# Kernel tuning notes

Hardware: AMD Instinct MI355X
Metric: run time of the kernel (lower is better)

The kernel has to match this reference:

```python
import jax, jax.numpy as jnp
import numpy as np

LN_EPS = 1e-5


def setup_inputs() -> dict:
    key = jax.random.key(0)
    k1, k2, k3 = jax.random.split(key, 3)
    B, T, D, H = 16, 512, 512, 1024
    x = jax.random.normal(k1, (B, T, D), dtype=jnp.float32)
    # nn.Linear weights: W in R^{2H x D}, U in R^{2H x H} (kaiming-ish scale)
    W_w = jax.random.normal(k2, (2 * H, D), dtype=jnp.float32) * (1.0 / np.sqrt(D))
    U_w = jax.random.normal(k3, (2 * H, H), dtype=jnp.float32) * (1.0 / np.sqrt(H))
    ln_gamma = jnp.ones((2 * H,), dtype=jnp.float32)
    ln_beta = jnp.zeros((2 * H,), dtype=jnp.float32)
    h0 = jnp.zeros((1, H), dtype=jnp.float32)
    return {"x": x, "W_w": W_w, "U_w": U_w, "ln_gamma": ln_gamma,
            "ln_beta": ln_beta, "h0": h0}


def _layernorm(w, gamma, beta):
    mu = jnp.mean(w, axis=-1, keepdims=True)
    var = jnp.mean(jnp.square(w - mu), axis=-1, keepdims=True)
    return (w - mu) * jax.lax.rsqrt(var + LN_EPS) * gamma + beta


def reference(x, W_w, U_w, ln_gamma, ln_beta, h0):
    # Input projection: w = x @ W^T -> [B, T, 2H], then LayerNorm over 2H
    w = jnp.einsum('btd,gd->btg', x, W_w)
    w = _layernorm(w, ln_gamma, ln_beta)

    B = x.shape[0]
    H = U_w.shape[1]
    ht0 = jnp.broadcast_to(h0, (B, H))
    U_t = U_w.T  # [H, 2H]

    def step(ht, wt):  # wt: [B, 2H]
        gates = wt + ht @ U_t
        at, zt = jnp.split(gates, 2, axis=1)
        zt = jax.nn.sigmoid(zt)
        hcand = jax.nn.relu(at)  # drop_mask = 1.0 in eval mode
        ht = zt * ht + (1.0 - zt) * hcand
        return ht, ht

    _, hs = jax.lax.scan(step, ht0, jnp.swapaxes(w, 0, 1))  # hs: [T, B, H]
    return jnp.swapaxes(hs, 0, 1)  # [B, T, H]
```

## Files before the change

kernel.cpp:

```cpp
#include <hip/hip_runtime.h>
#include <hip/hip_cooperative_groups.h>
#include <cmath>

typedef __bf16 bf16x8 __attribute__((ext_vector_type(8)));
typedef float floatx4 __attribute__((ext_vector_type(4)));
typedef unsigned ux4 __attribute__((ext_vector_type(4)));
typedef unsigned short u16;

#define B_ 16
#define T_ 512
#define D_ 512
#define H_ 1024
#define G_ 2048
#define BH (B_ * H_)
#define HP 1032

__global__ void cast_f32_bf16(const float* __restrict__ src, u16* __restrict__ dst, int n) {
  int i = blockIdx.x * blockDim.x + threadIdx.x;
  int stride = gridDim.x * blockDim.x;
  for (; i < n; i += stride) {
    __bf16 b = (__bf16)src[i];
    dst[i] = *reinterpret_cast<u16*>(&b);
  }
}

__launch_bounds__(256, 1)
__global__ void gemm_xW(const u16* __restrict__ xb, const u16* __restrict__ Wb,
                        float* __restrict__ w) {
  const int lane = threadIdx.x & 63;
  const int wv = threadIdx.x >> 6;
  const int rt0 = blockIdx.x * 16;
  const int bidx = rt0 >> 9;
  const int t0 = rt0 & 511;
  const int am = lane & 15;
  const int kq = lane >> 4;

  bf16x8 af[16];
  {
    const u16* xrow = xb + (size_t)(rt0 + am) * D_ + kq * 8;
#pragma unroll
    for (int kk = 0; kk < 16; ++kk)
      af[kk] = *reinterpret_cast<const bf16x8*>(xrow + kk * 32);
  }

#pragma unroll 1
  for (int nt = 0; nt < 32; ++nt) {
    const int n0 = wv * 512 + nt * 16;
    floatx4 acc = {0.f, 0.f, 0.f, 0.f};
    const u16* wrow = Wb + (size_t)(n0 + am) * D_ + kq * 8;
#pragma unroll
    for (int kk = 0; kk < 16; ++kk) {
      bf16x8 bfr = *reinterpret_cast<const bf16x8*>(wrow + kk * 32);
      acc = __builtin_amdgcn_mfma_f32_16x16x32_bf16(af[kk], bfr, acc, 0, 0, 0);
    }
#pragma unroll
    for (int i = 0; i < 4; ++i) {
      int m = kq * 4 + i;
      w[(size_t)((t0 + m) * 16 + bidx) * G_ + n0 + am] = acc[i];
    }
  }
}

__launch_bounds__(256, 1)
__global__ void layernorm_rows(float* __restrict__ w, const float* __restrict__ gamma,
                               const float* __restrict__ beta) {
  float* r = w + (size_t)blockIdx.x * G_;
  float v[8];
  float s = 0.f, ss = 0.f;
#pragma unroll
  for (int i = 0; i < 8; ++i) {
    v[i] = r[threadIdx.x + i * 256];
    s += v[i];
    ss += v[i] * v[i];
  }
#pragma unroll
  for (int d = 1; d < 64; d <<= 1) {
    s += __shfl_xor(s, d, 64);
    ss += __shfl_xor(ss, d, 64);
  }
  __shared__ float ls[4], lss[4];
  const int wv = threadIdx.x >> 6;
  if ((threadIdx.x & 63) == 0) { ls[wv] = s; lss[wv] = ss; }
  __syncthreads();
  float S = ls[0] + ls[1] + ls[2] + ls[3];
  float SS = lss[0] + lss[1] + lss[2] + lss[3];
  float mu = S * (1.f / 2048.f);
  float var = SS * (1.f / 2048.f) - mu * mu;
  float rs = rsqrtf(var + 1e-5f);
#pragma unroll
  for (int i = 0; i < 8; ++i) {
    int g = threadIdx.x + i * 256;
    r[g] = (v[i] - mu) * rs * gamma[g] + beta[g];
  }
}

__launch_bounds__(512, 1)
__global__ void ligru_scan(const float* __restrict__ w, const u16* __restrict__ Ub,
                           const float* __restrict__ h0, float* __restrict__ out,
                           unsigned* __restrict__ hbuf) {
  const int tid = threadIdx.x;
  const int lane = tid & 63;
  const int wv = tid >> 6;
  const int am = lane & 15;
  const int kq = lane >> 4;
  const int blk = blockIdx.x;
  const int j0 = blk * 32;
  const int jt = wv >> 1;
  const int kh = wv & 1;

  __shared__ u16 lds_h[16 * HP];
  __shared__ float lds_r[4][2][16][16];

  for (int i = tid; i < 8 * HP; i += 512) lds_h[8 * HP + i] = 0;

  const int grow = (am < 8) ? (j0 + 8 * jt + am) : (H_ + j0 + 8 * jt + (am - 8));

  bf16x8 uf[16];
  {
    const u16* urow = Ub + (size_t)grow * H_ + kh * 512 + kq * 8;
#pragma unroll
    for (int kk = 0; kk < 16; ++kk)
      uf[kk] = *reinterpret_cast<const bf16x8*>(urow + kk * 32);
  }

  const int ub = tid >> 5;
  const int jj = tid & 31;
  const int col = j0 + jj;
  const int scol = 4 * (tid & 255);
  const int sb = tid >> 8;
  float hreg = h0[col];
  float wa = __builtin_nontemporal_load(&w[(size_t)ub * G_ + col]);
  float wz = __builtin_nontemporal_load(&w[(size_t)ub * G_ + H_ + col]);

  {
    __bf16 hb = (__bf16)hreg;
    unsigned pk = ((unsigned)*reinterpret_cast<u16*>(&hb) << 16) | 1u;
    unsigned* pp = hbuf + ub * H_ + col;
    asm volatile("global_store_dword %0, %1, off sc0 sc1"
                 :: "v"(pp), "v"(pk) : "memory");
  }

  ux4 chv[4];
#define ISSUE_BUNDLE(base)                                                   \
  do {                                                                       \
    const unsigned* b_ = (base) + 4 * tid;                                   \
    asm volatile("global_load_dwordx4 %0, %4, off sc0 sc1\n\t"               \
                 "global_load_dwordx4 %1, %5, off sc0 sc1\n\t"               \
                 "global_load_dwordx4 %2, %6, off sc0 sc1\n\t"               \
                 "global_load_dwordx4 %3, %7, off sc0 sc1"                   \
                 : "=&v"(chv[0]), "=&v"(chv[1]), "=&v"(chv[2]), "=&v"(chv[3])\
                 : "v"(b_), "v"(b_ + 2048), "v"(b_ + 4096), "v"(b_ + 6144)   \
                 : "memory");                                                \
  } while (0)

  ISSUE_BUNDLE(hbuf);

  for (int t = 0; t < T_; ++t) {
    const unsigned tag = (unsigned)(t + 1);
#pragma unroll 1
    for (int g = 0; g < 2; ++g) {
      asm volatile("s_waitcnt vmcnt(0)"
                   : "+v"(chv[0]), "+v"(chv[1]), "+v"(chv[2]), "+v"(chv[3])
                   :: "memory");
      __builtin_amdgcn_sched_barrier(0);
      unsigned bad = 0;
#pragma unroll
      for (int c = 0; c < 4; ++c)
        bad |= ((chv[c].x ^ tag) | (chv[c].y ^ tag) |
                (chv[c].z ^ tag) | (chv[c].w ^ tag)) & 0xFFFFu;
      if (bad) {
        const unsigned* cb = hbuf + (size_t)(t & 1) * BH + g * 8192 + 4 * tid;
        unsigned rounds = 0;
        do {
          asm volatile(
              "global_load_dwordx4 %0, %4, off sc0 sc1\n\t"
              "global_load_dwordx4 %1, %5, off sc0 sc1\n\t"
              "global_load_dwordx4 %2, %6, off sc0 sc1\n\t"
              "global_load_dwordx4 %3, %7, off sc0 sc1\n\t"
              "s_waitcnt vmcnt(0)"
              : "=&v"(chv[0]), "=&v"(chv[1]), "=&v"(chv[2]), "=&v"(chv[3])
              : "v"(cb), "v"(cb + 2048), "v"(cb + 4096), "v"(cb + 6144)
              : "memory");
          bad = 0;
#pragma unroll
          for (int c = 0; c < 4; ++c)
            bad |= ((chv[c].x ^ tag) | (chv[c].y ^ tag) |
                    (chv[c].z ^ tag) | (chv[c].w ^ tag)) & 0xFFFFu;
        } while (bad && ++rounds < 2048u);
      }

#pragma unroll
      for (int c = 0; c < 4; ++c) {
        int b = 2 * c + sb;
        unsigned lo = (chv[c].x >> 16) | (chv[c].y & 0xFFFF0000u);
        unsigned hi = (chv[c].z >> 16) | (chv[c].w & 0xFFFF0000u);
        uint2 pk; pk.x = lo; pk.y = hi;
        *reinterpret_cast<uint2*>(&lds_h[b * HP + scol]) = pk;
      }
      asm volatile("s_waitcnt lgkmcnt(0)" ::: "memory");
      __builtin_amdgcn_s_barrier();
      __builtin_amdgcn_sched_barrier(0);

      floatx4 acc0 = {0, 0, 0, 0}, acc1 = {0, 0, 0, 0};
      {
        const u16* hb = &lds_h[am * HP + kh * 512 + kq * 8];
#pragma unroll
        for (int kk = 0; kk < 8; ++kk) {
          bf16x8 x0 = *reinterpret_cast<const bf16x8*>(hb + (kk + 0) * 32);
          bf16x8 x1 = *reinterpret_cast<const bf16x8*>(hb + (kk + 8) * 32);
          acc0 = __builtin_amdgcn_mfma_f32_16x16x32_bf16(x0, uf[kk + 0], acc0, 0, 0, 0);
          acc1 = __builtin_amdgcn_mfma_f32_16x16x32_bf16(x1, uf[kk + 8], acc1, 0, 0, 0);
        }
      }
      floatx4 acc = acc0 + acc1;

#pragma unroll
      for (int i = 0; i < 4; ++i)
        lds_r[jt][kh][kq * 4 + i][am] = acc[i];
      asm volatile("s_waitcnt lgkmcnt(0)" ::: "memory");
      __builtin_amdgcn_s_barrier();
      __builtin_amdgcn_sched_barrier(0);

      float wan = wa, wzn = wz;
      if (sb == g) {
        const int tl = jj >> 3, cc = jj & 7;
        const int mr = ub & 7;
        float a = lds_r[tl][0][mr][cc] + lds_r[tl][1][mr][cc] + wa;
        float z = lds_r[tl][0][mr][8 + cc] + lds_r[tl][1][mr][8 + cc] + wz;
        float zs = 1.f / (1.f + __expf(-z));
        float hn = zs * hreg + (1.f - zs) * fmaxf(a, 0.f);
        hreg = hn;
        __bf16 hb16 = (__bf16)hn;
        unsigned pk = ((unsigned)*reinterpret_cast<u16*>(&hb16) << 16) | (tag + 1u);
        unsigned* pp = hbuf + (size_t)((t + 1) & 1) * BH + ub * H_ + col;
        asm volatile("global_store_dword %0, %1, off sc0 sc1"
                     :: "v"(pp), "v"(pk) : "memory");
        __builtin_nontemporal_store(hn, &out[((size_t)ub * T_ + t) * H_ + col]);
        int tn = (t + 1 < T_) ? (t + 1) : t;
        const float* wt = w + (size_t)(tn * 16 + ub) * G_;
        wan = __builtin_nontemporal_load(&wt[col]);
        wzn = __builtin_nontemporal_load(&wt[H_ + col]);
      }
      wa = wan; wz = wzn;

      {
        int ntx = (g == 1) ? (t + 1) : t;
        const unsigned* nb = hbuf + (size_t)(ntx & 1) * BH + (g ^ 1) * 8192;
        ISSUE_BUNDLE(nb);
      }
    }
  }
#undef ISSUE_BUNDLE
}

extern "C" void kernel_launch(void* const* d_in, const int* in_sizes, int n_in,
                              void* d_out, int out_size, void* d_ws, size_t ws_size,
                              hipStream_t stream) {
  (void)in_sizes; (void)n_in; (void)out_size; (void)ws_size;
  const float* x = (const float*)d_in[0];
  const float* Ww = (const float*)d_in[1];
  const float* Uw = (const float*)d_in[2];
  const float* gamma = (const float*)d_in[3];
  const float* beta = (const float*)d_in[4];
  const float* h0 = (const float*)d_in[5];
  float* out = (float*)d_out;

  char* p = (char*)d_ws;
  u16* xb = (u16*)p;      p += (size_t)8192 * 512 * 2;
  u16* Wb = (u16*)p;      p += (size_t)2048 * 512 * 2;
  u16* Ub = (u16*)p;      p += (size_t)2048 * 1024 * 2;
  float* w = (float*)p;   p += (size_t)8192 * 2048 * 4;
  unsigned* hbuf = (unsigned*)p; p += (size_t)2 * BH * 4;

  hipMemsetAsync(hbuf, 0, (size_t)2 * BH * 4, stream);
  cast_f32_bf16<<<512, 256, 0, stream>>>(x, xb, 8192 * 512);
  cast_f32_bf16<<<256, 256, 0, stream>>>(Ww, Wb, 2048 * 512);
  cast_f32_bf16<<<256, 256, 0, stream>>>(Uw, Ub, 2048 * 1024);
  gemm_xW<<<512, 256, 0, stream>>>(xb, Wb, w);
  layernorm_rows<<<8192, 256, 0, stream>>>(w, gamma, beta);

  const float* wc = w;
  const u16* Ubc = Ub;
  void* args[5] = { (void*)&wc, (void*)&Ubc, (void*)&h0, (void*)&out, (void*)&hbuf };
  hipLaunchCooperativeKernel((void*)ligru_scan, dim3(32), dim3(512), args, 0, stream);
}
```

Measured before the change: 1.752 ms.

## Pin scan workgroups to one XCC and use L2-coherent polling loads

Launches 256 workgroups and elects the first XCC that gathers 32 of them to run the recurrent scan, while the other workgroups exit. With all 32 workers on one XCC, the h exchange can poll with sc0-only loads through the shared L2 instead of system-coherent sc0 sc1 loads. It falls back to sc0 sc1 loads after repeated stale reads. It also double-buffers the prefetch of w and issues it before the MFMA phase. The risk is that correctness of the sc0-only path depends on XCC co-location, and the election adds a startup cost plus extra launched blocks.

```diff
diff --git a/kernel.cpp b/kernel.cpp
--- a/kernel.cpp
+++ b/kernel.cpp
@@ -97,13 +97,28 @@
 __launch_bounds__(512, 1)
 __global__ void ligru_scan(const float* __restrict__ w, const u16* __restrict__ Ub,
                            const float* __restrict__ h0, float* __restrict__ out,
-                           unsigned* __restrict__ hbuf) {
+                           unsigned* __restrict__ hbuf, unsigned* __restrict__ elect) {
+  __shared__ unsigned s_role;
+  if (threadIdx.x == 0) {
+    unsigned xcc;
+    asm volatile("s_getreg_b32 %0, hwreg(HW_REG_XCC_ID)" : "=s"(xcc));
+    xcc &= 7u;
+    unsigned ticket = atomicAdd(&elect[xcc], 1u);
+    if (ticket == 31u) atomicCAS(&elect[8], 0u, xcc + 1u);
+    unsigned wn;
+    while ((wn = atomicAdd(&elect[8], 0u)) == 0u) __builtin_amdgcn_s_sleep(8);
+    s_role = (wn == xcc + 1u && ticket < 32u) ? ticket : 0xFFFFFFFFu;
+  }
+  __syncthreads();
+  const unsigned role = s_role;
+  if (role == 0xFFFFFFFFu) return;
+
   const int tid = threadIdx.x;
   const int lane = tid & 63;
   const int wv = tid >> 6;
   const int am = lane & 15;
   const int kq = lane >> 4;
-  const int blk = blockIdx.x;
+  const int blk = (int)role;
   const int j0 = blk * 32;
   const int jt = wv >> 1;
   const int kh = wv & 1;
@@ -129,8 +144,9 @@
   const int scol = 4 * (tid & 255);
   const int sb = tid >> 8;
   float hreg = h0[col];
-  float wa = __builtin_nontemporal_load(&w[(size_t)ub * G_ + col]);
-  float wz = __builtin_nontemporal_load(&w[(size_t)ub * G_ + H_ + col]);
+  float wa0 = __builtin_nontemporal_load(&w[(size_t)ub * G_ + col]);
+  float wz0 = __builtin_nontemporal_load(&w[(size_t)ub * G_ + H_ + col]);
+  float wa1 = 0.f, wz1 = 0.f;
 
   {
     __bf16 hb = (__bf16)hreg;
@@ -141,7 +157,19 @@
   }
 
   ux4 chv[4];
-#define ISSUE_BUNDLE(base)                                                   \
+  unsigned strikes = 0;
+#define ISSUE_SC0(base)                                                      \
+  do {                                                                       \
+    const unsigned* b_ = (base) + 4 * tid;                                   \
+    asm volatile("global_load_dwordx4 %0, %4, off sc0\n\t"                   \
+                 "global_load_dwordx4 %1, %5, off sc0\n\t"                   \
+                 "global_load_dwordx4 %2, %6, off sc0\n\t"                   \
+                 "global_load_dwordx4 %3, %7, off sc0"                       \
+                 : "=&v"(chv[0]), "=&v"(chv[1]), "=&v"(chv[2]), "=&v"(chv[3])\
+                 : "v"(b_), "v"(b_ + 2048), "v"(b_ + 4096), "v"(b_ + 6144)   \
+                 : "memory");                                                \
+  } while (0)
+#define ISSUE_SC01(base)                                                     \
   do {                                                                       \
     const unsigned* b_ = (base) + 4 * tid;                                   \
     asm volatile("global_load_dwordx4 %0, %4, off sc0 sc1\n\t"               \
@@ -153,7 +181,7 @@
                  : "memory");                                                \
   } while (0)
 
-  ISSUE_BUNDLE(hbuf);
+  ISSUE_SC0(hbuf);
 
   for (int t = 0; t < T_; ++t) {
     const unsigned tag = (unsigned)(t + 1);
@@ -168,25 +196,50 @@
       for (int c = 0; c < 4; ++c)
         bad |= ((chv[c].x ^ tag) | (chv[c].y ^ tag) |
                 (chv[c].z ^ tag) | (chv[c].w ^ tag)) & 0xFFFFu;
+      strikes += bad ? 1u : 0u;
       if (bad) {
         const unsigned* cb = hbuf + (size_t)(t & 1) * BH + g * 8192 + 4 * tid;
         unsigned rounds = 0;
         do {
-          asm volatile(
-              "global_load_dwordx4 %0, %4, off sc0 sc1\n\t"
-              "global_load_dwordx4 %1, %5, off sc0 sc1\n\t"
-              "global_load_dwordx4 %2, %6, off sc0 sc1\n\t"
-              "global_load_dwordx4 %3, %7, off sc0 sc1\n\t"
-              "s_waitcnt vmcnt(0)"
-              : "=&v"(chv[0]), "=&v"(chv[1]), "=&v"(chv[2]), "=&v"(chv[3])
-              : "v"(cb), "v"(cb + 2048), "v"(cb + 4096), "v"(cb + 6144)
-              : "memory");
+          if (rounds == 0) {
+            asm volatile(
+                "global_load_dwordx4 %0, %4, off sc0\n\t"
+                "global_load_dwordx4 %1, %5, off sc0\n\t"
+                "global_load_dwordx4 %2, %6, off sc0\n\t"
+                "global_load_dwordx4 %3, %7, off sc0\n\t"
+                "s_waitcnt vmcnt(0)"
+                : "=&v"(chv[0]), "=&v"(chv[1]), "=&v"(chv[2]), "=&v"(chv[3])
+                : "v"(cb), "v"(cb + 2048), "v"(cb + 4096), "v"(cb + 6144)
+                : "memory");
+          } else {
+            asm volatile(
+                "global_load_dwordx4 %0, %4, off sc0 sc1\n\t"
+                "global_load_dwordx4 %1, %5, off sc0 sc1\n\t"
+                "global_load_dwordx4 %2, %6, off sc0 sc1\n\t"
+                "global_load_dwordx4 %3, %7, off sc0 sc1\n\t"
+                "s_waitcnt vmcnt(0)"
+                : "=&v"(chv[0]), "=&v"(chv[1]), "=&v"(chv[2]), "=&v"(chv[3])
+                : "v"(cb), "v"(cb + 2048), "v"(cb + 4096), "v"(cb + 6144)
+                : "memory");
+          }
           bad = 0;
 #pragma unroll
           for (int c = 0; c < 4; ++c)
             bad |= ((chv[c].x ^ tag) | (chv[c].y ^ tag) |
                     (chv[c].z ^ tag) | (chv[c].w ^ tag)) & 0xFFFFu;
-        } while (bad && ++rounds < 2048u);
+        } while (bad && ++rounds < 4096u);
+      }
+
+      if (sb == g) {
+        int tn = (t + 1 < T_) ? (t + 1) : t;
+        const float* wt = w + (size_t)(tn * 16 + ub) * G_;
+        if (t & 1) {
+          wa0 = __builtin_nontemporal_load(&wt[col]);
+          wz0 = __builtin_nontemporal_load(&wt[H_ + col]);
+        } else {
+          wa1 = __builtin_nontemporal_load(&wt[col]);
+          wz1 = __builtin_nontemporal_load(&wt[H_ + col]);
+        }
       }
 
 #pragma unroll
@@ -221,12 +274,13 @@
       __builtin_amdgcn_s_barrier();
       __builtin_amdgcn_sched_barrier(0);
 
-      float wan = wa, wzn = wz;
       if (sb == g) {
         const int tl = jj >> 3, cc = jj & 7;
         const int mr = ub & 7;
-        float a = lds_r[tl][0][mr][cc] + lds_r[tl][1][mr][cc] + wa;
-        float z = lds_r[tl][0][mr][8 + cc] + lds_r[tl][1][mr][8 + cc] + wz;
+        float wai = (t & 1) ? wa1 : wa0;
+        float wzi = (t & 1) ? wz1 : wz0;
+        float a = lds_r[tl][0][mr][cc] + lds_r[tl][1][mr][cc] + wai;
+        float z = lds_r[tl][0][mr][8 + cc] + lds_r[tl][1][mr][8 + cc] + wzi;
         float zs = 1.f / (1.f + __expf(-z));
         float hn = zs * hreg + (1.f - zs) * fmaxf(a, 0.f);
         hreg = hn;
@@ -236,21 +290,17 @@
         asm volatile("global_store_dword %0, %1, off sc0 sc1"
                      :: "v"(pp), "v"(pk) : "memory");
         __builtin_nontemporal_store(hn, &out[((size_t)ub * T_ + t) * H_ + col]);
-        int tn = (t + 1 < T_) ? (t + 1) : t;
-        const float* wt = w + (size_t)(tn * 16 + ub) * G_;
-        wan = __builtin_nontemporal_load(&wt[col]);
-        wzn = __builtin_nontemporal_load(&wt[H_ + col]);
-      }
-      wa = wan; wz = wzn;
+      }
 
       {
         int ntx = (g == 1) ? (t + 1) : t;
         const unsigned* nb = hbuf + (size_t)(ntx & 1) * BH + (g ^ 1) * 8192;
-        ISSUE_BUNDLE(nb);
+        if (strikes < 16u) ISSUE_SC0(nb); else ISSUE_SC01(nb);
       }
     }
   }
-#undef ISSUE_BUNDLE
+#undef ISSUE_SC0
+#undef ISSUE_SC01
 }
 
 extern "C" void kernel_launch(void* const* d_in, const int* in_sizes, int n_in,
@@ -271,8 +321,9 @@
   u16* Ub = (u16*)p;      p += (size_t)2048 * 1024 * 2;
   float* w = (float*)p;   p += (size_t)8192 * 2048 * 4;
   unsigned* hbuf = (unsigned*)p; p += (size_t)2 * BH * 4;
-
-  hipMemsetAsync(hbuf, 0, (size_t)2 * BH * 4, stream);
+  unsigned* elect = (unsigned*)p; p += 64;
+
+  hipMemsetAsync(hbuf, 0, (size_t)2 * BH * 4 + 64, stream);
   cast_f32_bf16<<<512, 256, 0, stream>>>(x, xb, 8192 * 512);
   cast_f32_bf16<<<256, 256, 0, stream>>>(Ww, Wb, 2048 * 512);
   cast_f32_bf16<<<256, 256, 0, stream>>>(Uw, Ub, 2048 * 1024);
@@ -281,6 +332,7 @@
 
   const float* wc = w;
   const u16* Ubc = Ub;
-  void* args[5] = { (void*)&wc, (void*)&Ubc, (void*)&h0, (void*)&out, (void*)&hbuf };
-  hipLaunchCooperativeKernel((void*)ligru_scan, dim3(32), dim3(512), args, 0, stream);
-}
+  void* args[6] = { (void*)&wc, (void*)&Ubc, (void*)&h0, (void*)&out,
+                    (void*)&hbuf, (void*)&elect };
+  hipLaunchCooperativeKernel((void*)ligru_scan, dim3(256), dim3(512), args, 0, stream);
+}
```

Result: no change. 1.770 ms (+1.1%).

## Split scan across 64 blocks with dedicated loader warps and 4-batch groups

Applied to the files above, without the earlier changes.

Spreads the recurrent scan over 64 cooperative blocks of 16 hidden columns each instead of 32 blocks of 32. Each block now has four loader waves that poll the global h buffer, stage h into LDS and prefetch w values. The other four waves do the MFMA and gate work in four batch groups of 4 rows per timestep, padding the MFMA M-dimension. It also changes the LDS row pitch. The aim is more parallel U-weight residency and latency hiding for the cross-block h exchange. The cost is more sync phases per step and wasted MFMA rows.

```diff
diff --git a/kernel.cpp b/kernel.cpp
--- a/kernel.cpp
+++ b/kernel.cpp
@@ -13,7 +13,7 @@
 #define H_ 1024
 #define G_ 2048
 #define BH (B_ * H_)
-#define HP 1032
+#define HP 1058
 
 __global__ void cast_f32_bf16(const float* __restrict__ src, u16* __restrict__ dst, int n) {
   int i = blockIdx.x * blockDim.x + threadIdx.x;
@@ -104,153 +104,167 @@
   const int am = lane & 15;
   const int kq = lane >> 4;
   const int blk = blockIdx.x;
-  const int j0 = blk * 32;
-  const int jt = wv >> 1;
-  const int kh = wv & 1;
+  const int j0 = blk * 16;
+  const bool loader = (tid >= 256);
 
   __shared__ u16 lds_h[16 * HP];
-  __shared__ float lds_r[4][2][16][16];
-
-  for (int i = tid; i < 8 * HP; i += 512) lds_h[8 * HP + i] = 0;
-
-  const int grow = (am < 8) ? (j0 + 8 * jt + am) : (H_ + j0 + 8 * jt + (am - 8));
+  __shared__ float lds_r[2][2][16][16];
+  __shared__ float lds_w[2][4][2][16];
+
+  const int jt = wv & 1;
+  const int kh = (wv >> 1) & 1;
 
   bf16x8 uf[16];
-  {
+  if (!loader) {
+    const int grow = jt * H_ + j0 + am;
     const u16* urow = Ub + (size_t)grow * H_ + kh * 512 + kq * 8;
 #pragma unroll
     for (int kk = 0; kk < 16; ++kk)
       uf[kk] = *reinterpret_cast<const bf16x8*>(urow + kk * 32);
   }
 
-  const int ub = tid >> 5;
-  const int jj = tid & 31;
-  const int col = j0 + jj;
-  const int scol = 4 * (tid & 255);
-  const int sb = tid >> 8;
-  float hreg = h0[col];
-  float wa = __builtin_nontemporal_load(&w[(size_t)ub * G_ + col]);
-  float wz = __builtin_nontemporal_load(&w[(size_t)ub * G_ + H_ + col]);
-
-  {
+  const int ub = tid >> 4;
+  const int cl = tid & 15;
+  const int col = j0 + cl;
+  float hreg = 0.f;
+
+  const int li = tid & 255;
+  const int wb = (li >> 5) & 3;
+  const int wg = (li >> 4) & 1;
+  const int wc = li & 15;
+  ux4 chv0, chv1, chv2, chv3;
+  float wnx = 0.f;
+
+#define ISSUE_B(cb)                                                            \
+  asm volatile("global_load_dwordx4 %0, %4, off sc0 sc1\n\t"                   \
+               "global_load_dwordx4 %1, %5, off sc0 sc1\n\t"                   \
+               "global_load_dwordx4 %2, %6, off sc0 sc1\n\t"                   \
+               "global_load_dwordx4 %3, %7, off sc0 sc1"                       \
+               : "=&v"(chv0), "=&v"(chv1), "=&v"(chv2), "=&v"(chv3)            \
+               : "v"(cb), "v"((cb) + H_), "v"((cb) + 2 * H_), "v"((cb) + 3 * H_) \
+               : "memory")
+
+#define TAGCHK(tg)                                                             \
+  ((((chv0.x ^ (tg)) | (chv0.y ^ (tg)) | (chv0.z ^ (tg)) | (chv0.w ^ (tg)) |   \
+     (chv1.x ^ (tg)) | (chv1.y ^ (tg)) | (chv1.z ^ (tg)) | (chv1.w ^ (tg)) |   \
+     (chv2.x ^ (tg)) | (chv2.y ^ (tg)) | (chv2.z ^ (tg)) | (chv2.w ^ (tg)) |   \
+     (chv3.x ^ (tg)) | (chv3.y ^ (tg)) | (chv3.z ^ (tg)) | (chv3.w ^ (tg))) &  \
+    0xFFFFu))
+
+  if (!loader) {
+    hreg = h0[col];
     __bf16 hb = (__bf16)hreg;
     unsigned pk = ((unsigned)*reinterpret_cast<u16*>(&hb) << 16) | 1u;
     unsigned* pp = hbuf + ub * H_ + col;
     asm volatile("global_store_dword %0, %1, off sc0 sc1"
                  :: "v"(pp), "v"(pk) : "memory");
-  }
-
-  ux4 chv[4];
-#define ISSUE_BUNDLE(base)                                                   \
-  do {                                                                       \
-    const unsigned* b_ = (base) + 4 * tid;                                   \
-    asm volatile("global_load_dwordx4 %0, %4, off sc0 sc1\n\t"               \
-                 "global_load_dwordx4 %1, %5, off sc0 sc1\n\t"               \
-                 "global_load_dwordx4 %2, %6, off sc0 sc1\n\t"               \
-                 "global_load_dwordx4 %3, %7, off sc0 sc1"                   \
-                 : "=&v"(chv[0]), "=&v"(chv[1]), "=&v"(chv[2]), "=&v"(chv[3])\
-                 : "v"(b_), "v"(b_ + 2048), "v"(b_ + 4096), "v"(b_ + 6144)   \
-                 : "memory");                                                \
-  } while (0)
-
-  ISSUE_BUNDLE(hbuf);
-
+  } else {
+    if (li < 128) {
+      const float* ws = w + (size_t)wb * G_ + wg * H_ + j0 + wc;
+      asm volatile("global_load_dword %0, %1, off nt"
+                   : "=&v"(wnx) : "v"(ws) : "memory");
+    }
+    const unsigned* nb = hbuf + 4 * li;
+    ISSUE_B(nb);
+  }
+
+#pragma unroll 1
   for (int t = 0; t < T_; ++t) {
-    const unsigned tag = (unsigned)(t + 1);
 #pragma unroll 1
-    for (int g = 0; g < 2; ++g) {
-      asm volatile("s_waitcnt vmcnt(0)"
-                   : "+v"(chv[0]), "+v"(chv[1]), "+v"(chv[2]), "+v"(chv[3])
-                   :: "memory");
-      __builtin_amdgcn_sched_barrier(0);
-      unsigned bad = 0;
-#pragma unroll
-      for (int c = 0; c < 4; ++c)
-        bad |= ((chv[c].x ^ tag) | (chv[c].y ^ tag) |
-                (chv[c].z ^ tag) | (chv[c].w ^ tag)) & 0xFFFFu;
-      if (bad) {
-        const unsigned* cb = hbuf + (size_t)(t & 1) * BH + g * 8192 + 4 * tid;
-        unsigned rounds = 0;
-        do {
-          asm volatile(
-              "global_load_dwordx4 %0, %4, off sc0 sc1\n\t"
-              "global_load_dwordx4 %1, %5, off sc0 sc1\n\t"
-              "global_load_dwordx4 %2, %6, off sc0 sc1\n\t"
-              "global_load_dwordx4 %3, %7, off sc0 sc1\n\t"
-              "s_waitcnt vmcnt(0)"
-              : "=&v"(chv[0]), "=&v"(chv[1]), "=&v"(chv[2]), "=&v"(chv[3])
-              : "v"(cb), "v"(cb + 2048), "v"(cb + 4096), "v"(cb + 6144)
-              : "memory");
-          bad = 0;
-#pragma unroll
-          for (int c = 0; c < 4; ++c)
-            bad |= ((chv[c].x ^ tag) | (chv[c].y ^ tag) |
-                    (chv[c].z ^ tag) | (chv[c].w ^ tag)) & 0xFFFFu;
-        } while (bad && ++rounds < 2048u);
+    for (int g = 0; g < 4; ++g) {
+      const unsigned tag = (unsigned)(t + 1);
+      if (loader) {
+        asm volatile("s_waitcnt vmcnt(0)"
+                     : "+v"(chv0), "+v"(chv1), "+v"(chv2), "+v"(chv3), "+v"(wnx)
+                     :: "memory");
+        __builtin_amdgcn_sched_barrier(0);
+        unsigned bad = TAGCHK(tag);
+        if (bad) {
+          const unsigned* cb = hbuf + (size_t)(t & 1) * BH + 4 * g * H_ + 4 * li;
+          unsigned rounds = 0;
+          do {
+            ISSUE_B(cb);
+            asm volatile("s_waitcnt vmcnt(0)"
+                         : "+v"(chv0), "+v"(chv1), "+v"(chv2), "+v"(chv3)
+                         :: "memory");
+            bad = TAGCHK(tag);
+          } while (bad && ++rounds < 4096u);
+        }
+        if (li < 128) lds_w[g & 1][wb][wg][wc] = wnx;
+        {
+          unsigned lo, hi; uint2 pk2;
+          lo = (chv0.x >> 16) | (chv0.y & 0xFFFF0000u);
+          hi = (chv0.z >> 16) | (chv0.w & 0xFFFF0000u);
+          pk2.x = lo; pk2.y = hi;
+          *reinterpret_cast<uint2*>(&lds_h[(4 * g + 0) * HP + 4 * li]) = pk2;
+          lo = (chv1.x >> 16) | (chv1.y & 0xFFFF0000u);
+          hi = (chv1.z >> 16) | (chv1.w & 0xFFFF0000u);
+          pk2.x = lo; pk2.y = hi;
+          *reinterpret_cast<uint2*>(&lds_h[(4 * g + 1) * HP + 4 * li]) = pk2;
+          lo = (chv2.x >> 16) | (chv2.y & 0xFFFF0000u);
+          hi = (chv2.z >> 16) | (chv2.w & 0xFFFF0000u);
+          pk2.x = lo; pk2.y = hi;
+          *reinterpret_cast<uint2*>(&lds_h[(4 * g + 2) * HP + 4 * li]) = pk2;
+          lo = (chv3.x >> 16) | (chv3.y & 0xFFFF0000u);
+          hi = (chv3.z >> 16) | (chv3.w & 0xFFFF0000u);
+          pk2.x = lo; pk2.y = hi;
+          *reinterpret_cast<uint2*>(&lds_h[(4 * g + 3) * HP + 4 * li]) = pk2;
+        }
+        {
+          const int gn = (g + 1) & 3;
+          const int tb = (g == 3) ? (t + 1) : t;
+          const int tw = (g == 3) ? ((t + 1 < T_) ? t + 1 : t) : t;
+          if (li < 128) {
+            const float* ws = w + (size_t)(tw * 16 + 4 * gn + wb) * G_ +
+                              wg * H_ + j0 + wc;
+            asm volatile("global_load_dword %0, %1, off nt"
+                         : "=&v"(wnx) : "v"(ws) : "memory");
+          }
+          const unsigned* nb = hbuf + (size_t)(tb & 1) * BH + 4 * gn * H_ + 4 * li;
+          ISSUE_B(nb);
+        }
+        asm volatile("s_waitcnt lgkmcnt(0)" ::: "memory");
       }
-
-#pragma unroll
-      for (int c = 0; c < 4; ++c) {
-        int b = 2 * c + sb;
-        unsigned lo = (chv[c].x >> 16) | (chv[c].y & 0xFFFF0000u);
-        unsigned hi = (chv[c].z >> 16) | (chv[c].w & 0xFFFF0000u);
-        uint2 pk; pk.x = lo; pk.y = hi;
-        *reinterpret_cast<uint2*>(&lds_h[b * HP + scol]) = pk;
-      }
-      asm volatile("s_waitcnt lgkmcnt(0)" ::: "memory");
       __builtin_amdgcn_s_barrier();
       __builtin_amdgcn_sched_barrier(0);
 
-      floatx4 acc0 = {0, 0, 0, 0}, acc1 = {0, 0, 0, 0};
-      {
-        const u16* hb = &lds_h[am * HP + kh * 512 + kq * 8];
-#pragma unroll
-        for (int kk = 0; kk < 8; ++kk) {
-          bf16x8 x0 = *reinterpret_cast<const bf16x8*>(hb + (kk + 0) * 32);
-          bf16x8 x1 = *reinterpret_cast<const bf16x8*>(hb + (kk + 8) * 32);
-          acc0 = __builtin_amdgcn_mfma_f32_16x16x32_bf16(x0, uf[kk + 0], acc0, 0, 0, 0);
-          acc1 = __builtin_amdgcn_mfma_f32_16x16x32_bf16(x1, uf[kk + 8], acc1, 0, 0, 0);
+      if (!loader) {
+        const u16* hb = &lds_h[(4 * g + (am & 3)) * HP + kh * 512 + kq * 8];
+        floatx4 aa[4];
+        aa[0] = aa[1] = aa[2] = aa[3] = floatx4{0.f, 0.f, 0.f, 0.f};
+#pragma unroll
+        for (int kk = 0; kk < 16; ++kk) {
+          bf16x8 x = *reinterpret_cast<const bf16x8*>(hb + kk * 32);
+          aa[kk & 3] = __builtin_amdgcn_mfma_f32_16x16x32_bf16(x, uf[kk], aa[kk & 3], 0, 0, 0);
         }
+        floatx4 acc = (aa[0] + aa[1]) + (aa[2] + aa[3]);
+#pragma unroll
+        for (int i = 0; i < 4; ++i)
+          lds_r[jt][kh][kq * 4 + i][am] = acc[i];
+        asm volatile("s_waitcnt lgkmcnt(0)" ::: "memory");
       }
-      floatx4 acc = acc0 + acc1;
-
-#pragma unroll
-      for (int i = 0; i < 4; ++i)
-        lds_r[jt][kh][kq * 4 + i][am] = acc[i];
-      asm volatile("s_waitcnt lgkmcnt(0)" ::: "memory");
       __builtin_amdgcn_s_barrier();
       __builtin_amdgcn_sched_barrier(0);
 
-      float wan = wa, wzn = wz;
-      if (sb == g) {
-        const int tl = jj >> 3, cc = jj & 7;
-        const int mr = ub & 7;
-        float a = lds_r[tl][0][mr][cc] + lds_r[tl][1][mr][cc] + wa;
-        float z = lds_r[tl][0][mr][8 + cc] + lds_r[tl][1][mr][8 + cc] + wz;
+      if (!loader && wv == g) {
+        const int q = ub & 3;
+        float a = lds_r[0][0][q][cl] + lds_r[0][1][q][cl] + lds_w[g & 1][q][0][cl];
+        float z = lds_r[1][0][q][cl] + lds_r[1][1][q][cl] + lds_w[g & 1][q][1][cl];
         float zs = 1.f / (1.f + __expf(-z));
         float hn = zs * hreg + (1.f - zs) * fmaxf(a, 0.f);
         hreg = hn;
         __bf16 hb16 = (__bf16)hn;
-        unsigned pk = ((unsigned)*reinterpret_cast<u16*>(&hb16) << 16) | (tag + 1u);
+        unsigned pk = ((unsigned)*reinterpret_cast<u16*>(&hb16) << 16) |
+                      (unsigned)(t + 2);
         unsigned* pp = hbuf + (size_t)((t + 1) & 1) * BH + ub * H_ + col;
         asm volatile("global_store_dword %0, %1, off sc0 sc1"
                      :: "v"(pp), "v"(pk) : "memory");
         __builtin_nontemporal_store(hn, &out[((size_t)ub * T_ + t) * H_ + col]);
-        int tn = (t + 1 < T_) ? (t + 1) : t;
-        const float* wt = w + (size_t)(tn * 16 + ub) * G_;
-        wan = __builtin_nontemporal_load(&wt[col]);
-        wzn = __builtin_nontemporal_load(&wt[H_ + col]);
-      }
-      wa = wan; wz = wzn;
-
-      {
-        int ntx = (g == 1) ? (t + 1) : t;
-        const unsigned* nb = hbuf + (size_t)(ntx & 1) * BH + (g ^ 1) * 8192;
-        ISSUE_BUNDLE(nb);
       }
     }
   }
-#undef ISSUE_BUNDLE
+#undef ISSUE_B
+#undef TAGCHK
 }
 
 extern "C" void kernel_launch(void* const* d_in, const int* in_sizes, int n_in,
@@ -282,5 +296,5 @@
   const float* wc = w;
   const u16* Ubc = Ub;
   void* args[5] = { (void*)&wc, (void*)&Ubc, (void*)&h0, (void*)&out, (void*)&hbuf };
-  hipLaunchCooperativeKernel((void*)ligru_scan, dim3(32), dim3(512), args, 0, stream);
-}
+  hipLaunchCooperativeKernel((void*)ligru_scan, dim3(64), dim3(512), args, 0, stream);
+}
```

New measurement: 4.763 ms. 172% more time.
